# Kernel tuning notes

Hardware: AMD Instinct MI355X
Metric: run time of the kernel (lower is better)

## Reference

```python
import jax, jax.numpy as jnp
import numpy as np

T, B, C, H = 2048, 2, 1024, 16
D = C // H
SCALE = D ** -0.5
WSTD = C ** -0.5  # keep activations O(1) so softmax is not saturated


def setup_inputs() -> dict:
    key = jax.random.key(0)
    ks = jax.random.split(key, 6)
    return {
        "x": jax.random.normal(ks[0], (T, B, C), dtype=jnp.float32),
        "wq": jax.random.normal(ks[1], (C, C), dtype=jnp.float32) * WSTD,
        "wk": jax.random.normal(ks[2], (C, C), dtype=jnp.float32) * WSTD,
        "wv": jax.random.normal(ks[3], (C, C), dtype=jnp.float32) * WSTD,
        "wo": jax.random.normal(ks[4], (C, C), dtype=jnp.float32) * WSTD,
        "bo": jax.random.normal(ks[5], (C,), dtype=jnp.float32) * 0.02,
    }


def reference(x, wq, wk, wv, wo, bo):
    t, b, c = x.shape
    x2 = x.reshape(t * b, c)
    # SelfAttentionLinears: q scaled by head_dim^-0.5 inside the addmm
    q = (x2 @ wq) * SCALE
    k = x2 @ wk
    v = x2 @ wv
    # fairseq layout: (T, B*H, D) -> (B*H, T, D)
    q = q.reshape(t, b * H, D).transpose(1, 0, 2)
    k = k.reshape(t, b * H, D).transpose(1, 0, 2)
    v = v.reshape(t, b * H, D).transpose(1, 0, 2)
    # strided_bmm1: scores [B*H, T, T]
    scores = jnp.einsum('bqd,bkd->bqk', q, k)
    attn = jax.nn.softmax(scores, axis=-1)
    # strided_bmm2: context [B*H, T, D]
    ctx = jnp.einsum('bqk,bkd->bqd', attn, v)
    out = ctx.transpose(1, 0, 2).reshape(t, b, c)
    return out @ wo + bo
```

## Files before the change

kernel.cpp:

```cpp
#include <hip/hip_runtime.h>
#include <math.h>

#define T_DIM 2048
#define B_DIM 2
#define C_DIM 1024
#define H_DIM 16
#define D_DIM 64
#define M_DIM (T_DIM * B_DIM)
#define SCALE_Q 0.125f

typedef short short8 __attribute__((ext_vector_type(8)));
typedef float f32x4  __attribute__((ext_vector_type(4)));
typedef unsigned short ushort_t;

__device__ __forceinline__ unsigned short f2bf(float f) {
    unsigned int u = __builtin_bit_cast(unsigned int, f);
    u += 0x7FFFu + ((u >> 16) & 1u);
    return (unsigned short)(u >> 16);
}

__device__ __forceinline__ void gl_lds16(const void* g, void* l) {
    __builtin_amdgcn_global_load_lds(
        (const __attribute__((address_space(1))) void*)g,
        (__attribute__((address_space(3))) void*)l, 16, 0, 0);
}

__global__ __launch_bounds__(256) void prep(
    const float* __restrict__ x,
    const float* __restrict__ wq, const float* __restrict__ wk,
    const float* __restrict__ wv, const float* __restrict__ wo,
    ushort_t* __restrict__ xb,
    ushort_t* __restrict__ wqkv_t, ushort_t* __restrict__ wo_t)
{
    __shared__ float tile[64][65];
    const int tid = threadIdx.x;
    const int z   = blockIdx.z;

    if (z == 4) {
        const size_t base =
            ((size_t)(blockIdx.y * 16 + blockIdx.x)) * 16384 + (size_t)tid * 8;
#pragma unroll
        for (int j = 0; j < 8; ++j) {
            const size_t i = base + (size_t)j * 2048;
            const float4 v0 = *(const float4*)&x[i];
            const float4 v1 = *(const float4*)&x[i + 4];
            ushort_t o[8] = {f2bf(v0.x), f2bf(v0.y), f2bf(v0.z), f2bf(v0.w),
                             f2bf(v1.x), f2bf(v1.y), f2bf(v1.z), f2bf(v1.w)};
            *(uint4*)&xb[i] = *(uint4*)o;
        }
        return;
    }

    const int k0 = blockIdx.x * 64;
    const int n0 = blockIdx.y * 64;
    const float* src = (z == 0) ? wq : (z == 1) ? wk : (z == 2) ? wv : wo;
    ushort_t* dst = (z < 3) ? (wqkv_t + (size_t)z * C_DIM * C_DIM) : wo_t;

    const int r = tid >> 4;
    const int c = (tid & 15) * 4;
#pragma unroll
    for (int i = 0; i < 4; ++i) {
        const float4 v = *(const float4*)&src[(size_t)(k0 + r + i * 16) * C_DIM + n0 + c];
        *(float4*)&tile[r + i * 16][c] = v;
    }
    __syncthreads();
#pragma unroll
    for (int i = 0; i < 4; ++i) {
        const int r2 = r + i * 16;
        ushort4 o;
        o.x = f2bf(tile[c + 0][r2]); o.y = f2bf(tile[c + 1][r2]);
        o.z = f2bf(tile[c + 2][r2]); o.w = f2bf(tile[c + 3][r2]);
        *(ushort4*)&dst[(size_t)(n0 + r2) * C_DIM + k0 + c] = o;
    }
}

__global__ __launch_bounds__(256) void qkv_mfma(
    const ushort_t* __restrict__ xb, const ushort_t* __restrict__ wt,
    ushort_t* __restrict__ q_ws, ushort_t* __restrict__ k_ws,
    ushort_t* __restrict__ v_ws)
{
    __shared__ ushort_t lds[18432];
    ushort_t* As = lds;
    ushort_t* Bs = lds + 4096;

    const int tid  = threadIdx.x;
    const int n0   = blockIdx.x * 128;
    const int m0   = blockIdx.y * 128;
    const int w    = tid >> 6;
    const int lane = tid & 63;
    const int l16  = lane & 15;
    const int quad = lane >> 4;
    const int wm   = (w >> 1) * 64;
    const int wn   = (w & 1) * 64;

    const int o0 = tid * 8, o1 = o0 + 2048;
    const ushort_t* a0 = xb + (size_t)(m0 + (o0 >> 5)) * C_DIM + (o0 & 31);
    const ushort_t* a1 = xb + (size_t)(m0 + (o1 >> 5)) * C_DIM + (o1 & 31);
    const ushort_t* b0 = wt + (size_t)(n0 + (o0 >> 5)) * C_DIM + (o0 & 31);
    const ushort_t* b1 = wt + (size_t)(n0 + (o1 >> 5)) * C_DIM + (o1 & 31);

    f32x4 acc[4][4] = {};

    for (int k0 = 0; k0 < C_DIM; k0 += 32) {
        __syncthreads();
        gl_lds16(a0 + k0, As + o0);
        gl_lds16(a1 + k0, As + o1);
        gl_lds16(b0 + k0, Bs + o0);
        gl_lds16(b1 + k0, Bs + o1);
        __syncthreads();

        short8 af[4], bf[4];
#pragma unroll
        for (int mi = 0; mi < 4; ++mi)
            af[mi] = *(const short8*)&As[(wm + mi * 16 + l16) * 32 + quad * 8];
#pragma unroll
        for (int ni = 0; ni < 4; ++ni)
            bf[ni] = *(const short8*)&Bs[(wn + ni * 16 + l16) * 32 + quad * 8];
#pragma unroll
        for (int mi = 0; mi < 4; ++mi)
#pragma unroll
            for (int ni = 0; ni < 4; ++ni)
                acc[mi][ni] = __builtin_amdgcn_mfma_f32_16x16x32_bf16(
                    af[mi], bf[ni], acc[mi][ni], 0, 0, 0);
    }

    __syncthreads();
    ushort_t* Ep = lds + w * 4608;

    const int mat = n0 >> 10;
    const int cb  = (n0 & 1023) + wn;
    const int h   = cb >> 6;
    ushort_t* dst = (mat == 0) ? q_ws : (mat == 1) ? k_ws : v_ws;
    const float sc = (mat == 0) ? SCALE_Q : 1.0f;

#pragma unroll
    for (int mi = 0; mi < 4; ++mi)
#pragma unroll
        for (int ni = 0; ni < 4; ++ni)
#pragma unroll
            for (int r = 0; r < 4; ++r)
                Ep[(mi * 16 + quad * 4 + r) * 72 + ni * 16 + l16] =
                    f2bf(acc[mi][ni][r] * sc);

    const int rq = lane >> 3;
    const int c8 = (lane & 7) * 8;
#pragma unroll
    for (int p = 0; p < 8; ++p) {
        const int row = p * 8 + rq;
        const uint4 val = *(const uint4*)&Ep[row * 72 + c8];
        const int m = m0 + wm + row;
        const int t = m >> 1, b = m & 1;
        *(uint4*)&dst[((size_t)(b * H_DIM + h) * T_DIM + t) * D_DIM + c8] = val;
    }
}

__global__ __launch_bounds__(256) void v_transpose(
    const ushort_t* __restrict__ vn, ushort_t* __restrict__ vt)
{
    __shared__ ushort_t tile[64][72];
    const int tid = threadIdx.x;
    const int t0  = blockIdx.x * 64;
    const int bh  = blockIdx.y;
    const int r   = tid >> 3;
    const int c   = (tid & 7) * 8;
#pragma unroll
    for (int i = 0; i < 2; ++i)
        *(uint4*)&tile[r + i * 32][c] =
            *(const uint4*)&vn[((size_t)bh * T_DIM + t0 + r + i * 32) * D_DIM + c];
    __syncthreads();
#pragma unroll
    for (int i = 0; i < 2; ++i) {
        const int rd = r + i * 32;
        ushort_t o[8];
#pragma unroll
        for (int j = 0; j < 8; ++j) o[j] = tile[c + j][rd];
        *(uint4*)&vt[((size_t)bh * D_DIM + rd) * T_DIM + t0 + c] = *(uint4*)o;
    }
}

__global__ __launch_bounds__(256) void attn_mfma(
    const ushort_t* __restrict__ q, const ushort_t* __restrict__ k,
    const ushort_t* __restrict__ v, ushort_t* __restrict__ ctx)
{
    __shared__ ushort_t Ks [64][72];
    __shared__ ushort_t Vts[64][72];
    __shared__ ushort_t Ps [64][72];

    const int tid  = threadIdx.x;
    const int bh   = blockIdx.x;
    const int q0   = blockIdx.y * 64;
    const int w    = tid >> 6;
    const int lane = tid & 63;
    const int l16  = lane & 15;
    const int quad = lane >> 4;

    const int r0 = tid >> 3,         c80 = (tid & 7) * 8;
    const int r1 = (tid + 256) >> 3;
    const ushort_t* kbase = k + (size_t)bh * T_DIM * D_DIM;
    const ushort_t* vbase = v + (size_t)bh * D_DIM * T_DIM;

    short8 aq0, aq1;
    {
        const ushort_t* qrow = q + ((size_t)bh * T_DIM + q0 + 16 * w + l16) * D_DIM;
        aq0 = *(const short8*)(qrow + quad * 8);
        aq1 = *(const short8*)(qrow + 32 + quad * 8);
    }

    short8 vones;
#pragma unroll
    for (int j = 0; j < 8; ++j) vones[j] = (short)0x3F80;

    f32x4 O[4] = {};
    f32x4 Osum = {};

    const ushort_t* kp0 = kbase + (size_t)r0 * D_DIM + c80;
    const ushort_t* kp1 = kbase + (size_t)r1 * D_DIM + c80;
    const ushort_t* vp0 = vbase + (size_t)r0 * T_DIM + c80;
    const ushort_t* vp1 = vbase + (size_t)r1 * T_DIM + c80;
    uint4 kr0 = *(const uint4*)kp0;  kp0 += 64 * D_DIM;
    uint4 kr1 = *(const uint4*)kp1;  kp1 += 64 * D_DIM;
    uint4 vr0 = *(const uint4*)vp0;  vp0 += 64;
    uint4 vr1 = *(const uint4*)vp1;  vp1 += 64;

    const float LOG2E = 1.44269504f;
    const float SHIFT = 8.0f * 1.44269504f;

    for (int kt = 0; kt < 32; ++kt) {
        __syncthreads();
        *(uint4*)&Ks[r0][c80]  = kr0;
        *(uint4*)&Ks[r1][c80]  = kr1;
        *(uint4*)&Vts[r0][c80] = vr0;
        *(uint4*)&Vts[r1][c80] = vr1;
        if (kt + 1 < 32) {
            kr0 = *(const uint4*)kp0;  kp0 += 64 * D_DIM;
            kr1 = *(const uint4*)kp1;  kp1 += 64 * D_DIM;
            vr0 = *(const uint4*)vp0;  vp0 += 64;
            vr1 = *(const uint4*)vp1;  vp1 += 64;
        }
        __syncthreads();

        f32x4 S[4];
#pragma unroll
        for (int nt = 0; nt < 4; ++nt) {
            const short8 b0 = *(const short8*)&Ks[nt * 16 + l16][quad * 8];
            const short8 b1 = *(const short8*)&Ks[nt * 16 + l16][32 + quad * 8];
            f32x4 s = (f32x4){0.f, 0.f, 0.f, 0.f};
            s = __builtin_amdgcn_mfma_f32_16x16x32_bf16(aq0, b0, s, 0, 0, 0);
            s = __builtin_amdgcn_mfma_f32_16x16x32_bf16(aq1, b1, s, 0, 0, 0);
            S[nt] = s;
        }

#pragma unroll
        for (int nt = 0; nt < 4; ++nt)
#pragma unroll
            for (int r = 0; r < 4; ++r) {
                union { float f; ushort2 h; } cv;
                cv.f = exp2f(fmaf(S[nt][r], LOG2E, -SHIFT));
                Ps[16 * w + quad * 4 + r][nt * 16 + l16] = cv.h.y;
            }

        const short8 ap0 = *(const short8*)&Ps[16 * w + l16][quad * 8];
        const short8 ap1 = *(const short8*)&Ps[16 * w + l16][32 + quad * 8];

        Osum = __builtin_amdgcn_mfma_f32_16x16x32_bf16(ap0, vones, Osum, 0, 0, 0);
        Osum = __builtin_amdgcn_mfma_f32_16x16x32_bf16(ap1, vones, Osum, 0, 0, 0);

#pragma unroll
        for (int nt = 0; nt < 4; ++nt) {
            const short8 b0 = *(const short8*)&Vts[nt * 16 + l16][quad * 8];
            const short8 b1 = *(const short8*)&Vts[nt * 16 + l16][32 + quad * 8];
            O[nt] = __builtin_amdgcn_mfma_f32_16x16x32_bf16(ap0, b0, O[nt], 0, 0, 0);
            O[nt] = __builtin_amdgcn_mfma_f32_16x16x32_bf16(ap1, b1, O[nt], 0, 0, 0);
        }
    }

    const int b = bh >> 4;
    const int h = bh & 15;
#pragma unroll
    for (int r = 0; r < 4; ++r) {
        const float inv = 1.0f / Osum[r];
        const int row = q0 + 16 * w + quad * 4 + r;
#pragma unroll
        for (int nt = 0; nt < 4; ++nt)
            ctx[((size_t)row * B_DIM + b) * C_DIM + h * 64 + nt * 16 + l16] =
                f2bf(O[nt][r] * inv);
    }
}

__global__ __launch_bounds__(256) void out_mfma(
    const ushort_t* __restrict__ ctx, const ushort_t* __restrict__ wot,
    const float* __restrict__ bo, float* __restrict__ out)
{
    __shared__ ushort_t As[128 * 32];
    __shared__ ushort_t Bs[64 * 32];

    const int tid  = threadIdx.x;
    const int n0   = blockIdx.x * 64;
    const int m0   = blockIdx.y * 128;
    const int w    = tid >> 6;
    const int lane = tid & 63;
    const int l16  = lane & 15;
    const int quad = lane >> 4;
    const int wm   = (w >> 1) * 64;
    const int wn   = (w & 1) * 32;

    const int o0 = tid * 8, o1 = o0 + 2048;
    const ushort_t* a0 = ctx + (size_t)(m0 + (o0 >> 5)) * C_DIM + (o0 & 31);
    const ushort_t* a1 = ctx + (size_t)(m0 + (o1 >> 5)) * C_DIM + (o1 & 31);
    const ushort_t* b0 = wot + (size_t)(n0 + (o0 >> 5)) * C_DIM + (o0 & 31);

    f32x4 acc[4][2] = {};

    for (int k0 = 0; k0 < C_DIM; k0 += 32) {
        __syncthreads();
        gl_lds16(a0 + k0, As + o0);
        gl_lds16(a1 + k0, As + o1);
        gl_lds16(b0 + k0, Bs + o0);
        __syncthreads();

        short8 af[4], bf[2];
#pragma unroll
        for (int mi = 0; mi < 4; ++mi)
            af[mi] = *(const short8*)&As[(wm + mi * 16 + l16) * 32 + quad * 8];
#pragma unroll
        for (int ni = 0; ni < 2; ++ni)
            bf[ni] = *(const short8*)&Bs[(wn + ni * 16 + l16) * 32 + quad * 8];
#pragma unroll
        for (int mi = 0; mi < 4; ++mi)
#pragma unroll
            for (int ni = 0; ni < 2; ++ni)
                acc[mi][ni] = __builtin_amdgcn_mfma_f32_16x16x32_bf16(
                    af[mi], bf[ni], acc[mi][ni], 0, 0, 0);
    }

#pragma unroll
    for (int ni = 0; ni < 2; ++ni) {
        const int n = n0 + wn + ni * 16 + l16;
        const float bias = bo[n];
#pragma unroll
        for (int mi = 0; mi < 4; ++mi) {
            const int mb = m0 + wm + mi * 16 + quad * 4;
#pragma unroll
            for (int r = 0; r < 4; ++r)
                out[(size_t)(mb + r) * C_DIM + n] = acc[mi][ni][r] + bias;
        }
    }
}

extern "C" void kernel_launch(void* const* d_in, const int* in_sizes, int n_in,
                              void* d_out, int out_size, void* d_ws, size_t ws_size,
                              hipStream_t stream)
{
    const float* x  = (const float*)d_in[0];
    const float* wq = (const float*)d_in[1];
    const float* wk = (const float*)d_in[2];
    const float* wv = (const float*)d_in[3];
    const float* wo = (const float*)d_in[4];
    const float* bo = (const float*)d_in[5];
    float* out = (float*)d_out;

    const size_t CC  = (size_t)C_DIM * C_DIM;
    const size_t MC  = (size_t)M_DIM * C_DIM;
    ushort_t* xb     = (ushort_t*)d_ws;
    ushort_t* wqkv_t = xb + MC;
    ushort_t* wo_t   = wqkv_t + 3 * CC;
    ushort_t* q_ws   = wo_t + CC;
    ushort_t* k_ws   = q_ws + MC;
    ushort_t* v_nat  = k_ws + MC;
    ushort_t* v_t    = v_nat + MC;
    ushort_t* ctx    = v_t + MC;

    hipLaunchKernelGGL(prep, dim3(16, 16, 5), dim3(256), 0, stream,
                       x, wq, wk, wv, wo, xb, wqkv_t, wo_t);
    hipLaunchKernelGGL(qkv_mfma, dim3(24, 32), dim3(256), 0, stream,
                       xb, wqkv_t, q_ws, k_ws, v_nat);
    hipLaunchKernelGGL(v_transpose, dim3(32, 32), dim3(256), 0, stream,
                       v_nat, v_t);
    hipLaunchKernelGGL(attn_mfma, dim3(32, 32), dim3(256), 0, stream,
                       q_ws, k_ws, v_t, ctx);
    hipLaunchKernelGGL(out_mfma, dim3(16, 32), dim3(256), 0, stream,
                       ctx, wo_t, bo, out);
}
```

Measured before the change: 212.7 us.

## Fuse V transpose into QKV epilogue and deepen GEMM K-step to 64

The separate v_transpose kernel is removed. The QKV GEMM epilogue now writes V directly in transposed (bh, d, t) layout from its LDS staging tile, which saves a launch and a round trip of V through global memory. Both the QKV and output GEMMs now stage 64-wide K slices per barrier pair instead of 32, which halves the number of synchronisations. The cost is more LDS per block, and the transposed epilogue reads LDS with strided, bank-conflict-prone accesses.

```diff
diff --git a/kernel.cpp b/kernel.cpp
--- a/kernel.cpp
+++ b/kernel.cpp
@@ -77,11 +77,11 @@
 __global__ __launch_bounds__(256) void qkv_mfma(
     const ushort_t* __restrict__ xb, const ushort_t* __restrict__ wt,
     ushort_t* __restrict__ q_ws, ushort_t* __restrict__ k_ws,
-    ushort_t* __restrict__ v_ws)
+    ushort_t* __restrict__ v_t)
 {
     __shared__ ushort_t lds[18432];
     ushort_t* As = lds;
-    ushort_t* Bs = lds + 4096;
+    ushort_t* Bs = lds + 8192;
 
     const int tid  = threadIdx.x;
     const int n0   = blockIdx.x * 128;
@@ -93,35 +93,44 @@
     const int wm   = (w >> 1) * 64;
     const int wn   = (w & 1) * 64;
 
-    const int o0 = tid * 8, o1 = o0 + 2048;
-    const ushort_t* a0 = xb + (size_t)(m0 + (o0 >> 5)) * C_DIM + (o0 & 31);
-    const ushort_t* a1 = xb + (size_t)(m0 + (o1 >> 5)) * C_DIM + (o1 & 31);
-    const ushort_t* b0 = wt + (size_t)(n0 + (o0 >> 5)) * C_DIM + (o0 & 31);
-    const ushort_t* b1 = wt + (size_t)(n0 + (o1 >> 5)) * C_DIM + (o1 & 31);
+    const int srow = tid >> 3;
+    const int sc8  = (tid & 7) * 8;
+    const ushort_t* aP[4];
+    const ushort_t* bP[4];
+#pragma unroll
+    for (int j = 0; j < 4; ++j) {
+        aP[j] = xb + (size_t)(m0 + srow + j * 32) * C_DIM + sc8;
+        bP[j] = wt + (size_t)(n0 + srow + j * 32) * C_DIM + sc8;
+    }
+    const int ldso = tid * 8;
 
     f32x4 acc[4][4] = {};
 
-    for (int k0 = 0; k0 < C_DIM; k0 += 32) {
-        __syncthreads();
-        gl_lds16(a0 + k0, As + o0);
-        gl_lds16(a1 + k0, As + o1);
-        gl_lds16(b0 + k0, Bs + o0);
-        gl_lds16(b1 + k0, Bs + o1);
-        __syncthreads();
-
-        short8 af[4], bf[4];
-#pragma unroll
-        for (int mi = 0; mi < 4; ++mi)
-            af[mi] = *(const short8*)&As[(wm + mi * 16 + l16) * 32 + quad * 8];
-#pragma unroll
-        for (int ni = 0; ni < 4; ++ni)
-            bf[ni] = *(const short8*)&Bs[(wn + ni * 16 + l16) * 32 + quad * 8];
-#pragma unroll
-        for (int mi = 0; mi < 4; ++mi)
+    for (int k0 = 0; k0 < C_DIM; k0 += 64) {
+        __syncthreads();
+#pragma unroll
+        for (int j = 0; j < 4; ++j) {
+            gl_lds16(aP[j] + k0, As + ldso + j * 2048);
+            gl_lds16(bP[j] + k0, Bs + ldso + j * 2048);
+        }
+        __syncthreads();
+
+#pragma unroll
+        for (int s = 0; s < 2; ++s) {
+            short8 af[4], bf[4];
+#pragma unroll
+            for (int mi = 0; mi < 4; ++mi)
+                af[mi] = *(const short8*)&As[(wm + mi * 16 + l16) * 64 + s * 32 + quad * 8];
 #pragma unroll
             for (int ni = 0; ni < 4; ++ni)
-                acc[mi][ni] = __builtin_amdgcn_mfma_f32_16x16x32_bf16(
-                    af[mi], bf[ni], acc[mi][ni], 0, 0, 0);
+                bf[ni] = *(const short8*)&Bs[(wn + ni * 16 + l16) * 64 + s * 32 + quad * 8];
+#pragma unroll
+            for (int mi = 0; mi < 4; ++mi)
+#pragma unroll
+                for (int ni = 0; ni < 4; ++ni)
+                    acc[mi][ni] = __builtin_amdgcn_mfma_f32_16x16x32_bf16(
+                        af[mi], bf[ni], acc[mi][ni], 0, 0, 0);
+        }
     }
 
     __syncthreads();
@@ -130,7 +139,6 @@
     const int mat = n0 >> 10;
     const int cb  = (n0 & 1023) + wn;
     const int h   = cb >> 6;
-    ushort_t* dst = (mat == 0) ? q_ws : (mat == 1) ? k_ws : v_ws;
     const float sc = (mat == 0) ? SCALE_Q : 1.0f;
 
 #pragma unroll
@@ -142,39 +150,33 @@
                 Ep[(mi * 16 + quad * 4 + r) * 72 + ni * 16 + l16] =
                     f2bf(acc[mi][ni][r] * sc);
 
-    const int rq = lane >> 3;
-    const int c8 = (lane & 7) * 8;
-#pragma unroll
-    for (int p = 0; p < 8; ++p) {
-        const int row = p * 8 + rq;
-        const uint4 val = *(const uint4*)&Ep[row * 72 + c8];
-        const int m = m0 + wm + row;
-        const int t = m >> 1, b = m & 1;
-        *(uint4*)&dst[((size_t)(b * H_DIM + h) * T_DIM + t) * D_DIM + c8] = val;
-    }
-}
-
-__global__ __launch_bounds__(256) void v_transpose(
-    const ushort_t* __restrict__ vn, ushort_t* __restrict__ vt)
-{
-    __shared__ ushort_t tile[64][72];
-    const int tid = threadIdx.x;
-    const int t0  = blockIdx.x * 64;
-    const int bh  = blockIdx.y;
-    const int r   = tid >> 3;
-    const int c   = (tid & 7) * 8;
-#pragma unroll
-    for (int i = 0; i < 2; ++i)
-        *(uint4*)&tile[r + i * 32][c] =
-            *(const uint4*)&vn[((size_t)bh * T_DIM + t0 + r + i * 32) * D_DIM + c];
-    __syncthreads();
-#pragma unroll
-    for (int i = 0; i < 2; ++i) {
-        const int rd = r + i * 32;
-        ushort_t o[8];
-#pragma unroll
-        for (int j = 0; j < 8; ++j) o[j] = tile[c + j][rd];
-        *(uint4*)&vt[((size_t)bh * D_DIM + rd) * T_DIM + t0 + c] = *(uint4*)o;
+    if (mat == 2) {
+        const int dq  = lane >> 3;
+        const int b   = (lane >> 2) & 1;
+        const int tc  = lane & 3;
+        const int tg0 = (m0 + wm) >> 1;
+#pragma unroll
+        for (int p = 0; p < 8; ++p) {
+            const int d = p * 8 + dq;
+            ushort_t o[8];
+#pragma unroll
+            for (int i = 0; i < 8; ++i)
+                o[i] = Ep[(2 * (tc * 8 + i) + b) * 72 + d];
+            *(uint4*)&v_t[((size_t)(b * H_DIM + h) * D_DIM + d) * T_DIM + tg0 + tc * 8] =
+                *(uint4*)o;
+        }
+    } else {
+        ushort_t* dst = (mat == 0) ? q_ws : k_ws;
+        const int rq = lane >> 3;
+        const int c8 = (lane & 7) * 8;
+#pragma unroll
+        for (int p = 0; p < 8; ++p) {
+            const int row = p * 8 + rq;
+            const uint4 val = *(const uint4*)&Ep[row * 72 + c8];
+            const int m = m0 + wm + row;
+            const int t = m >> 1, b = m & 1;
+            *(uint4*)&dst[((size_t)(b * H_DIM + h) * T_DIM + t) * D_DIM + c8] = val;
+        }
     }
 }
 
@@ -291,8 +293,8 @@
     const ushort_t* __restrict__ ctx, const ushort_t* __restrict__ wot,
     const float* __restrict__ bo, float* __restrict__ out)
 {
-    __shared__ ushort_t As[128 * 32];
-    __shared__ ushort_t Bs[64 * 32];
+    __shared__ ushort_t As[128 * 64];
+    __shared__ ushort_t Bs[64 * 64];
 
     const int tid  = threadIdx.x;
     const int n0   = blockIdx.x * 64;
@@ -304,33 +306,46 @@
     const int wm   = (w >> 1) * 64;
     const int wn   = (w & 1) * 32;
 
-    const int o0 = tid * 8, o1 = o0 + 2048;
-    const ushort_t* a0 = ctx + (size_t)(m0 + (o0 >> 5)) * C_DIM + (o0 & 31);
-    const ushort_t* a1 = ctx + (size_t)(m0 + (o1 >> 5)) * C_DIM + (o1 & 31);
-    const ushort_t* b0 = wot + (size_t)(n0 + (o0 >> 5)) * C_DIM + (o0 & 31);
+    const int srow = tid >> 3;
+    const int sc8  = (tid & 7) * 8;
+    const ushort_t* aP[4];
+#pragma unroll
+    for (int j = 0; j < 4; ++j)
+        aP[j] = ctx + (size_t)(m0 + srow + j * 32) * C_DIM + sc8;
+    const ushort_t* bP[2];
+#pragma unroll
+    for (int j = 0; j < 2; ++j)
+        bP[j] = wot + (size_t)(n0 + srow + j * 32) * C_DIM + sc8;
+    const int ldso = tid * 8;
 
     f32x4 acc[4][2] = {};
 
-    for (int k0 = 0; k0 < C_DIM; k0 += 32) {
-        __syncthreads();
-        gl_lds16(a0 + k0, As + o0);
-        gl_lds16(a1 + k0, As + o1);
-        gl_lds16(b0 + k0, Bs + o0);
-        __syncthreads();
-
-        short8 af[4], bf[2];
-#pragma unroll
-        for (int mi = 0; mi < 4; ++mi)
-            af[mi] = *(const short8*)&As[(wm + mi * 16 + l16) * 32 + quad * 8];
-#pragma unroll
-        for (int ni = 0; ni < 2; ++ni)
-            bf[ni] = *(const short8*)&Bs[(wn + ni * 16 + l16) * 32 + quad * 8];
-#pragma unroll
-        for (int mi = 0; mi < 4; ++mi)
+    for (int k0 = 0; k0 < C_DIM; k0 += 64) {
+        __syncthreads();
+#pragma unroll
+        for (int j = 0; j < 4; ++j)
+            gl_lds16(aP[j] + k0, As + ldso + j * 2048);
+#pragma unroll
+        for (int j = 0; j < 2; ++j)
+            gl_lds16(bP[j] + k0, Bs + ldso + j * 2048);
+        __syncthreads();
+
+#pragma unroll
+        for (int s = 0; s < 2; ++s) {
+            short8 af[4], bf[2];
+#pragma unroll
+            for (int mi = 0; mi < 4; ++mi)
+                af[mi] = *(const short8*)&As[(wm + mi * 16 + l16) * 64 + s * 32 + quad * 8];
 #pragma unroll
             for (int ni = 0; ni < 2; ++ni)
-                acc[mi][ni] = __builtin_amdgcn_mfma_f32_16x16x32_bf16(
-                    af[mi], bf[ni], acc[mi][ni], 0, 0, 0);
+                bf[ni] = *(const short8*)&Bs[(wn + ni * 16 + l16) * 64 + s * 32 + quad * 8];
+#pragma unroll
+            for (int mi = 0; mi < 4; ++mi)
+#pragma unroll
+                for (int ni = 0; ni < 2; ++ni)
+                    acc[mi][ni] = __builtin_amdgcn_mfma_f32_16x16x32_bf16(
+                        af[mi], bf[ni], acc[mi][ni], 0, 0, 0);
+        }
     }
 
 #pragma unroll
@@ -366,16 +381,13 @@
     ushort_t* wo_t   = wqkv_t + 3 * CC;
     ushort_t* q_ws   = wo_t + CC;
     ushort_t* k_ws   = q_ws + MC;
-    ushort_t* v_nat  = k_ws + MC;
-    ushort_t* v_t    = v_nat + MC;
+    ushort_t* v_t    = k_ws + MC;
     ushort_t* ctx    = v_t + MC;
 
     hipLaunchKernelGGL(prep, dim3(16, 16, 5), dim3(256), 0, stream,
                        x, wq, wk, wv, wo, xb, wqkv_t, wo_t);
     hipLaunchKernelGGL(qkv_mfma, dim3(24, 32), dim3(256), 0, stream,
-                       xb, wqkv_t, q_ws, k_ws, v_nat);
-    hipLaunchKernelGGL(v_transpose, dim3(32, 32), dim3(256), 0, stream,
-                       v_nat, v_t);
+                       xb, wqkv_t, q_ws, k_ws, v_t);
     hipLaunchKernelGGL(attn_mfma, dim3(32, 32), dim3(256), 0, stream,
                        q_ws, k_ws, v_t, ctx);
     hipLaunchKernelGGL(out_mfma, dim3(16, 32), dim3(256), 0, stream,
```

Result: slower. 219.8 us (+3.4%).

## Give each attention wave two 16-row query tiles with 128-thread blocks

Applied to the files above, without the earlier changes.

The attention kernel drops from four waves per block to two, and each wave now handles 32 query rows as two 16-row MFMA tiles instead of one. Every K and V fragment read from LDS is reused across both row tiles, which halves the LDS fragment traffic per MFMA and gives each wave more independent MFMAs to interleave. In exchange each thread holds more registers (accumulators, scores, loads), which may lower occupancy, and each block has fewer waves to hide the global load and barrier latency.

```diff
diff --git a/kernel.cpp b/kernel.cpp
--- a/kernel.cpp
+++ b/kernel.cpp
@@ -178,7 +178,7 @@
     }
 }
 
-__global__ __launch_bounds__(256) void attn_mfma(
+__global__ __launch_bounds__(128) void attn_mfma(
     const ushort_t* __restrict__ q, const ushort_t* __restrict__ k,
     const ushort_t* __restrict__ v, ushort_t* __restrict__ ctx)
 {
@@ -193,98 +193,126 @@
     const int lane = tid & 63;
     const int l16  = lane & 15;
     const int quad = lane >> 4;
-
-    const int r0 = tid >> 3,         c80 = (tid & 7) * 8;
-    const int r1 = (tid + 256) >> 3;
+    const int wr   = 32 * w;
+
+    const int r0  = tid >> 3;
+    const int c80 = (tid & 7) * 8;
     const ushort_t* kbase = k + (size_t)bh * T_DIM * D_DIM;
     const ushort_t* vbase = v + (size_t)bh * D_DIM * T_DIM;
 
-    short8 aq0, aq1;
-    {
-        const ushort_t* qrow = q + ((size_t)bh * T_DIM + q0 + 16 * w + l16) * D_DIM;
-        aq0 = *(const short8*)(qrow + quad * 8);
-        aq1 = *(const short8*)(qrow + 32 + quad * 8);
+    short8 aq[2][2];
+#pragma unroll
+    for (int mi = 0; mi < 2; ++mi) {
+        const ushort_t* qrow =
+            q + ((size_t)bh * T_DIM + q0 + wr + mi * 16 + l16) * D_DIM;
+        aq[mi][0] = *(const short8*)(qrow + quad * 8);
+        aq[mi][1] = *(const short8*)(qrow + 32 + quad * 8);
     }
 
     short8 vones;
 #pragma unroll
     for (int j = 0; j < 8; ++j) vones[j] = (short)0x3F80;
 
-    f32x4 O[4] = {};
-    f32x4 Osum = {};
-
-    const ushort_t* kp0 = kbase + (size_t)r0 * D_DIM + c80;
-    const ushort_t* kp1 = kbase + (size_t)r1 * D_DIM + c80;
-    const ushort_t* vp0 = vbase + (size_t)r0 * T_DIM + c80;
-    const ushort_t* vp1 = vbase + (size_t)r1 * T_DIM + c80;
-    uint4 kr0 = *(const uint4*)kp0;  kp0 += 64 * D_DIM;
-    uint4 kr1 = *(const uint4*)kp1;  kp1 += 64 * D_DIM;
-    uint4 vr0 = *(const uint4*)vp0;  vp0 += 64;
-    uint4 vr1 = *(const uint4*)vp1;  vp1 += 64;
+    f32x4 O[2][4] = {};
+    f32x4 Osum[2] = {};
+
+    const ushort_t* kp[4];
+    const ushort_t* vp[4];
+    uint4 kr[4], vr[4];
+#pragma unroll
+    for (int j = 0; j < 4; ++j) {
+        kp[j] = kbase + (size_t)(r0 + j * 16) * D_DIM + c80;
+        vp[j] = vbase + (size_t)(r0 + j * 16) * T_DIM + c80;
+        kr[j] = *(const uint4*)kp[j];  kp[j] += 64 * D_DIM;
+        vr[j] = *(const uint4*)vp[j];  vp[j] += 64;
+    }
 
     const float LOG2E = 1.44269504f;
     const float SHIFT = 8.0f * 1.44269504f;
 
     for (int kt = 0; kt < 32; ++kt) {
         __syncthreads();
-        *(uint4*)&Ks[r0][c80]  = kr0;
-        *(uint4*)&Ks[r1][c80]  = kr1;
-        *(uint4*)&Vts[r0][c80] = vr0;
-        *(uint4*)&Vts[r1][c80] = vr1;
+#pragma unroll
+        for (int j = 0; j < 4; ++j) {
+            *(uint4*)&Ks [r0 + j * 16][c80] = kr[j];
+            *(uint4*)&Vts[r0 + j * 16][c80] = vr[j];
+        }
         if (kt + 1 < 32) {
-            kr0 = *(const uint4*)kp0;  kp0 += 64 * D_DIM;
-            kr1 = *(const uint4*)kp1;  kp1 += 64 * D_DIM;
-            vr0 = *(const uint4*)vp0;  vp0 += 64;
-            vr1 = *(const uint4*)vp1;  vp1 += 64;
-        }
-        __syncthreads();
-
-        f32x4 S[4];
+#pragma unroll
+            for (int j = 0; j < 4; ++j) {
+                kr[j] = *(const uint4*)kp[j];  kp[j] += 64 * D_DIM;
+                vr[j] = *(const uint4*)vp[j];  vp[j] += 64;
+            }
+        }
+        __syncthreads();
+
+        f32x4 S[2][4];
 #pragma unroll
         for (int nt = 0; nt < 4; ++nt) {
             const short8 b0 = *(const short8*)&Ks[nt * 16 + l16][quad * 8];
             const short8 b1 = *(const short8*)&Ks[nt * 16 + l16][32 + quad * 8];
-            f32x4 s = (f32x4){0.f, 0.f, 0.f, 0.f};
-            s = __builtin_amdgcn_mfma_f32_16x16x32_bf16(aq0, b0, s, 0, 0, 0);
-            s = __builtin_amdgcn_mfma_f32_16x16x32_bf16(aq1, b1, s, 0, 0, 0);
-            S[nt] = s;
-        }
-
-#pragma unroll
-        for (int nt = 0; nt < 4; ++nt)
-#pragma unroll
-            for (int r = 0; r < 4; ++r) {
-                union { float f; ushort2 h; } cv;
-                cv.f = exp2f(fmaf(S[nt][r], LOG2E, -SHIFT));
-                Ps[16 * w + quad * 4 + r][nt * 16 + l16] = cv.h.y;
+#pragma unroll
+            for (int mi = 0; mi < 2; ++mi) {
+                f32x4 s = (f32x4){0.f, 0.f, 0.f, 0.f};
+                s = __builtin_amdgcn_mfma_f32_16x16x32_bf16(aq[mi][0], b0, s, 0, 0, 0);
+                s = __builtin_amdgcn_mfma_f32_16x16x32_bf16(aq[mi][1], b1, s, 0, 0, 0);
+                S[mi][nt] = s;
             }
-
-        const short8 ap0 = *(const short8*)&Ps[16 * w + l16][quad * 8];
-        const short8 ap1 = *(const short8*)&Ps[16 * w + l16][32 + quad * 8];
-
-        Osum = __builtin_amdgcn_mfma_f32_16x16x32_bf16(ap0, vones, Osum, 0, 0, 0);
-        Osum = __builtin_amdgcn_mfma_f32_16x16x32_bf16(ap1, vones, Osum, 0, 0, 0);
+        }
+
+#pragma unroll
+        for (int mi = 0; mi < 2; ++mi)
+#pragma unroll
+            for (int nt = 0; nt < 4; ++nt)
+#pragma unroll
+                for (int r = 0; r < 4; ++r) {
+                    union { float f; ushort2 h; } cv;
+                    cv.f = exp2f(fmaf(S[mi][nt][r], LOG2E, -SHIFT));
+                    Ps[wr + mi * 16 + quad * 4 + r][nt * 16 + l16] = cv.h.y;
+                }
+
+        short8 ap[2][2];
+#pragma unroll
+        for (int mi = 0; mi < 2; ++mi) {
+            ap[mi][0] = *(const short8*)&Ps[wr + mi * 16 + l16][quad * 8];
+            ap[mi][1] = *(const short8*)&Ps[wr + mi * 16 + l16][32 + quad * 8];
+        }
+
+#pragma unroll
+        for (int mi = 0; mi < 2; ++mi) {
+            Osum[mi] = __builtin_amdgcn_mfma_f32_16x16x32_bf16(
+                ap[mi][0], vones, Osum[mi], 0, 0, 0);
+            Osum[mi] = __builtin_amdgcn_mfma_f32_16x16x32_bf16(
+                ap[mi][1], vones, Osum[mi], 0, 0, 0);
+        }
 
 #pragma unroll
         for (int nt = 0; nt < 4; ++nt) {
             const short8 b0 = *(const short8*)&Vts[nt * 16 + l16][quad * 8];
             const short8 b1 = *(const short8*)&Vts[nt * 16 + l16][32 + quad * 8];
-            O[nt] = __builtin_amdgcn_mfma_f32_16x16x32_bf16(ap0, b0, O[nt], 0, 0, 0);
-            O[nt] = __builtin_amdgcn_mfma_f32_16x16x32_bf16(ap1, b1, O[nt], 0, 0, 0);
+#pragma unroll
+            for (int mi = 0; mi < 2; ++mi) {
+                O[mi][nt] = __builtin_amdgcn_mfma_f32_16x16x32_bf16(
+                    ap[mi][0], b0, O[mi][nt], 0, 0, 0);
+                O[mi][nt] = __builtin_amdgcn_mfma_f32_16x16x32_bf16(
+                    ap[mi][1], b1, O[mi][nt], 0, 0, 0);
+            }
         }
     }
 
     const int b = bh >> 4;
     const int h = bh & 15;
 #pragma unroll
-    for (int r = 0; r < 4; ++r) {
-        const float inv = 1.0f / Osum[r];
-        const int row = q0 + 16 * w + quad * 4 + r;
-#pragma unroll
-        for (int nt = 0; nt < 4; ++nt)
-            ctx[((size_t)row * B_DIM + b) * C_DIM + h * 64 + nt * 16 + l16] =
-                f2bf(O[nt][r] * inv);
-    }
+    for (int mi = 0; mi < 2; ++mi)
+#pragma unroll
+        for (int r = 0; r < 4; ++r) {
+            const float inv = 1.0f / Osum[mi][r];
+            const int row = q0 + wr + mi * 16 + quad * 4 + r;
+#pragma unroll
+            for (int nt = 0; nt < 4; ++nt)
+                ctx[((size_t)row * B_DIM + b) * C_DIM + h * 64 + nt * 16 + l16] =
+                    f2bf(O[mi][nt][r] * inv);
+        }
 }
 
 __global__ __launch_bounds__(256) void out_mfma(
@@ -376,7 +404,7 @@
                        xb, wqkv_t, q_ws, k_ws, v_nat);
     hipLaunchKernelGGL(v_transpose, dim3(32, 32), dim3(256), 0, stream,
                        v_nat, v_t);
-    hipLaunchKernelGGL(attn_mfma, dim3(32, 32), dim3(256), 0, stream,
+    hipLaunchKernelGGL(attn_mfma, dim3(32, 32), dim3(128), 0, stream,
                        q_ws, k_ws, v_t, ctx);
     hipLaunchKernelGGL(out_mfma, dim3(16, 32), dim3(256), 0, stream,
                        ctx, wo_t, bo, out);
```

New measurement: 320.2 us. 50.6% more time.

## Keep attention probabilities in registers via transposed S and fp16 PV MFMA

Applied to the files above, without the earlier changes.

Computes S transposed (K as the A operand, Q as B) so each lane's score accumulator matches the B-operand layout of a 16x16x16 f16 MFMA. The exponentiated probabilities then feed the PV product directly from registers, with no LDS round trip through the Ps buffer and the __syncthreads-free write/read that went with it. V is converted to fp16 in the transpose kernel, the row sum is accumulated in scalar registers plus two shuffles instead of an extra MFMA against ones, and context stores become 4-wide vectors. In exchange there are twice as many smaller-K MFMAs for PV, and fp16 probabilities and V are less accurate in range than bf16.

```diff
diff --git a/kernel.cpp b/kernel.cpp
--- a/kernel.cpp
+++ b/kernel.cpp
@@ -11,12 +11,19 @@
 
 typedef short short8 __attribute__((ext_vector_type(8)));
 typedef float f32x4  __attribute__((ext_vector_type(4)));
+typedef _Float16 half4 __attribute__((ext_vector_type(4)));
 typedef unsigned short ushort_t;
 
 __device__ __forceinline__ unsigned short f2bf(float f) {
     unsigned int u = __builtin_bit_cast(unsigned int, f);
     u += 0x7FFFu + ((u >> 16) & 1u);
     return (unsigned short)(u >> 16);
+}
+
+__device__ __forceinline__ unsigned short bf2h(unsigned short b) {
+    const float f = __builtin_bit_cast(float, (unsigned int)b << 16);
+    const _Float16 h = (_Float16)f;
+    return __builtin_bit_cast(unsigned short, h);
 }
 
 __device__ __forceinline__ void gl_lds16(const void* g, void* l) {
@@ -173,7 +180,7 @@
         const int rd = r + i * 32;
         ushort_t o[8];
 #pragma unroll
-        for (int j = 0; j < 8; ++j) o[j] = tile[c + j][rd];
+        for (int j = 0; j < 8; ++j) o[j] = bf2h(tile[c + j][rd]);
         *(uint4*)&vt[((size_t)bh * D_DIM + rd) * T_DIM + t0 + c] = *(uint4*)o;
     }
 }
@@ -184,7 +191,6 @@
 {
     __shared__ ushort_t Ks [64][72];
     __shared__ ushort_t Vts[64][72];
-    __shared__ ushort_t Ps [64][72];
 
     const int tid  = threadIdx.x;
     const int bh   = blockIdx.x;
@@ -206,12 +212,8 @@
         aq1 = *(const short8*)(qrow + 32 + quad * 8);
     }
 
-    short8 vones;
-#pragma unroll
-    for (int j = 0; j < 8; ++j) vones[j] = (short)0x3F80;
-
     f32x4 O[4] = {};
-    f32x4 Osum = {};
+    float lacc = 0.f;
 
     const ushort_t* kp0 = kbase + (size_t)r0 * D_DIM + c80;
     const ushort_t* kp1 = kbase + (size_t)r1 * D_DIM + c80;
@@ -241,49 +243,51 @@
 
         f32x4 S[4];
 #pragma unroll
-        for (int nt = 0; nt < 4; ++nt) {
-            const short8 b0 = *(const short8*)&Ks[nt * 16 + l16][quad * 8];
-            const short8 b1 = *(const short8*)&Ks[nt * 16 + l16][32 + quad * 8];
+        for (int mt = 0; mt < 4; ++mt) {
+            const short8 a0 = *(const short8*)&Ks[mt * 16 + l16][quad * 8];
+            const short8 a1 = *(const short8*)&Ks[mt * 16 + l16][32 + quad * 8];
             f32x4 s = (f32x4){0.f, 0.f, 0.f, 0.f};
-            s = __builtin_amdgcn_mfma_f32_16x16x32_bf16(aq0, b0, s, 0, 0, 0);
-            s = __builtin_amdgcn_mfma_f32_16x16x32_bf16(aq1, b1, s, 0, 0, 0);
-            S[nt] = s;
-        }
-
-#pragma unroll
-        for (int nt = 0; nt < 4; ++nt)
+            s = __builtin_amdgcn_mfma_f32_16x16x32_bf16(a0, aq0, s, 0, 0, 0);
+            s = __builtin_amdgcn_mfma_f32_16x16x32_bf16(a1, aq1, s, 0, 0, 0);
+            S[mt] = s;
+        }
+
+        half4 pf[4];
+#pragma unroll
+        for (int mt = 0; mt < 4; ++mt)
 #pragma unroll
             for (int r = 0; r < 4; ++r) {
-                union { float f; ushort2 h; } cv;
-                cv.f = exp2f(fmaf(S[nt][r], LOG2E, -SHIFT));
-                Ps[16 * w + quad * 4 + r][nt * 16 + l16] = cv.h.y;
+                const float p = exp2f(fmaf(S[mt][r], LOG2E, -SHIFT));
+                lacc += p;
+                pf[mt][r] = (_Float16)p;
             }
 
-        const short8 ap0 = *(const short8*)&Ps[16 * w + l16][quad * 8];
-        const short8 ap1 = *(const short8*)&Ps[16 * w + l16][32 + quad * 8];
-
-        Osum = __builtin_amdgcn_mfma_f32_16x16x32_bf16(ap0, vones, Osum, 0, 0, 0);
-        Osum = __builtin_amdgcn_mfma_f32_16x16x32_bf16(ap1, vones, Osum, 0, 0, 0);
-
-#pragma unroll
-        for (int nt = 0; nt < 4; ++nt) {
-            const short8 b0 = *(const short8*)&Vts[nt * 16 + l16][quad * 8];
-            const short8 b1 = *(const short8*)&Vts[nt * 16 + l16][32 + quad * 8];
-            O[nt] = __builtin_amdgcn_mfma_f32_16x16x32_bf16(ap0, b0, O[nt], 0, 0, 0);
-            O[nt] = __builtin_amdgcn_mfma_f32_16x16x32_bf16(ap1, b1, O[nt], 0, 0, 0);
-        }
-    }
+#pragma unroll
+        for (int dt = 0; dt < 4; ++dt) {
+#pragma unroll
+            for (int mt = 0; mt < 4; ++mt) {
+                const half4 av =
+                    *(const half4*)&Vts[dt * 16 + l16][mt * 16 + quad * 4];
+                O[dt] = __builtin_amdgcn_mfma_f32_16x16x16f16(
+                    av, pf[mt], O[dt], 0, 0, 0);
+            }
+        }
+    }
+
+    lacc += __shfl_xor(lacc, 16);
+    lacc += __shfl_xor(lacc, 32);
+    const float inv = 1.0f / lacc;
 
     const int b = bh >> 4;
     const int h = bh & 15;
-#pragma unroll
-    for (int r = 0; r < 4; ++r) {
-        const float inv = 1.0f / Osum[r];
-        const int row = q0 + 16 * w + quad * 4 + r;
-#pragma unroll
-        for (int nt = 0; nt < 4; ++nt)
-            ctx[((size_t)row * B_DIM + b) * C_DIM + h * 64 + nt * 16 + l16] =
-                f2bf(O[nt][r] * inv);
+    const int row = q0 + 16 * w + l16;
+    ushort_t* cbase = ctx + ((size_t)row * B_DIM + b) * C_DIM + h * 64;
+#pragma unroll
+    for (int dt = 0; dt < 4; ++dt) {
+        ushort4 o;
+        o.x = f2bf(O[dt][0] * inv); o.y = f2bf(O[dt][1] * inv);
+        o.z = f2bf(O[dt][2] * inv); o.w = f2bf(O[dt][3] * inv);
+        *(ushort4*)&cbase[dt * 16 + quad * 4] = o;
     }
 }
 
```

Measured after the change: 216.0 us. No clear change (+1.6%).
